# Optimization experiments

Hardware: AMD Instinct MI355X
Metric: run time of the kernel (lower is better)

## Reference

```python
import jax, jax.numpy as jnp
import numpy as np

DIM = 768
HEADS = 12
DIM_HEAD = 64
INNER = HEADS * DIM_HEAD
L = 256
EPS = 1e-08


def setup_inputs() -> dict:
    key = jax.random.key(0)
    k1, k2, k3, k4 = jax.random.split(key, 4)
    x = jax.random.normal(k1, (2, 4096, DIM), dtype=jnp.float32)
    # Linear weights stored torch-style: (out_features, in_features)
    w_qkv = jax.random.normal(k2, (3 * INNER, DIM), dtype=jnp.float32) * (DIM ** -0.5)
    w_out = jax.random.normal(k3, (DIM, INNER), dtype=jnp.float32) * (INNER ** -0.5)
    b_out = jax.random.normal(k4, (DIM,), dtype=jnp.float32) * 0.01
    # learned per-head log-scale temperature, init log2(L^2 - L)
    scale = jnp.full((HEADS,), np.log2(L * L - L), dtype=jnp.float32)
    return {"x": x, "w_qkv": w_qkv, "w_out": w_out, "b_out": b_out, "scale": scale}


def reference(x, w_qkv, w_out, b_out, scale):
    b, n, d = x.shape
    h, dh = HEADS, DIM_HEAD
    qkv = x @ w_qkv.T                                   # [b, n, 3*inner]
    q, k, v = jnp.split(qkv, 3, axis=-1)
    # [b, n, h, dh] -> [b, h, n, dh]
    q, k, v = (t.reshape(b, n, h, dh).transpose(0, 2, 1, 3) for t in (q, k, v))
    # Faithful to source: L2 norm over the HEADS axis (dim=1), then rsqrt
    q = q * jax.lax.rsqrt(jnp.linalg.norm(q, axis=1, keepdims=True) + EPS)
    k = k * jax.lax.rsqrt(jnp.linalg.norm(k, axis=1, keepdims=True) + EPS)
    dots = jnp.einsum('bhid,bhjd->bhij', q, k)          # [b, h, n, n]
    scores = jax.nn.softmax(dots / scale[:, None, None], axis=-1)
    out = jnp.einsum('bhij,bhjd->bhid', scores, v)      # [b, h, n, dh]
    out = out.transpose(0, 2, 1, 3).reshape(b, n, h * dh)
    return out @ w_out.T + b_out
```

## Files before the change

kernel.cpp:

```cpp
#include <hip/hip_runtime.h>
#include <hip/hip_bf16.h>

#define DIMX   768
#define HEADS  12
#define DH     64
#define INNER  768
#define NQKV   2304
#define SEQ    4096
#define BATCH  2
#define ROWS   (BATCH*SEQ)
#define EPSF   1e-8f
#define LOG2E  1.4426950408889634f

typedef __bf16 bf16x8 __attribute__((ext_vector_type(8)));
typedef float  f32x4  __attribute__((ext_vector_type(4)));
typedef float  f32x16 __attribute__((ext_vector_type(16)));
typedef unsigned u32x2 __attribute__((ext_vector_type(2)));

__device__ __forceinline__ unsigned short f2bf(float f) {
    unsigned int u = __float_as_uint(f);
    unsigned int r = ((u >> 16) & 1u) + 0x7FFFu;
    return (unsigned short)((u + r) >> 16);
}
__device__ __forceinline__ float bf2f(unsigned short u) {
    return __builtin_bit_cast(float, (unsigned)u << 16);
}
__device__ __forceinline__ unsigned pkbf(float a, float b) {
    unsigned short la = __builtin_bit_cast(unsigned short, (__bf16)a);
    unsigned short lb = __builtin_bit_cast(unsigned short, (__bf16)b);
    return (unsigned)la | ((unsigned)lb << 16);
}

__device__ __forceinline__ void gload_lds16(const void* g, void* l) {
    __builtin_amdgcn_global_load_lds(
        (const __attribute__((address_space(1))) void*)g,
        (__attribute__((address_space(3))) void*)l, 16, 0, 0);
}

__global__ __launch_bounds__(256) void cast_f32_bf16(
    const float* __restrict__ src, unsigned short* __restrict__ dst, int n)
{
    int i = (blockIdx.x * 256 + threadIdx.x) * 4;
    if (i + 3 < n) {
        float4 v = *reinterpret_cast<const float4*>(src + i);
        ushort4 o;
        o.x = f2bf(v.x); o.y = f2bf(v.y); o.z = f2bf(v.z); o.w = f2bf(v.w);
        *reinterpret_cast<ushort4*>(dst + i) = o;
    }
}

template<bool BF16OUT>
__global__ __launch_bounds__(256) void gemm_bt_kernel(
    const unsigned short* __restrict__ A,
    const unsigned short* __restrict__ B,
    void* __restrict__ Cv,
    const float* __restrict__ bias,
    int M, int N, int K, int bmx)
{
    __shared__ unsigned short shA[128][64];
    __shared__ unsigned short shB[128][64];

    const int xcd = blockIdx.x & 7;
    const int idx = blockIdx.x >> 3;
    const int bm0 = (xcd * bmx + (idx % bmx)) * 128;
    const int bn0 = (idx / bmx) * 128;
    const int tid = threadIdx.x;
    const int lane = tid & 63;
    const int wid  = tid >> 6;
    const int l15  = lane & 15;
    const int l4   = lane >> 4;
    const int wr   = wid >> 1;
    const int wc   = wid & 1;
    const int srow = lane >> 3;
    const int scol = (lane & 7) * 8;

    f32x4 acc[4][4];
    #pragma unroll
    for (int i = 0; i < 4; ++i)
        #pragma unroll
        for (int j = 0; j < 4; ++j)
            acc[i][j] = (f32x4){0.f, 0.f, 0.f, 0.f};

    const int nkt = K >> 6;
    for (int kt = 0; kt < nkt; ++kt) {
        const int k0 = kt << 6;
        __syncthreads();
        #pragma unroll
        for (int j = 0; j < 4; ++j) {
            int row = wid * 32 + j * 8;
            gload_lds16(&A[(size_t)(bm0 + row + srow) * K + k0 + scol], &shA[row][0]);
            gload_lds16(&B[(size_t)(bn0 + row + srow) * K + k0 + scol], &shB[row][0]);
        }
        __syncthreads();
        #pragma unroll
        for (int ks = 0; ks < 2; ++ks) {
            bf16x8 af[4], bfr[4];
            #pragma unroll
            for (int mf = 0; mf < 4; ++mf)
                af[mf] = *reinterpret_cast<const bf16x8*>(&shA[wr * 64 + mf * 16 + l15][ks * 32 + l4 * 8]);
            #pragma unroll
            for (int nf = 0; nf < 4; ++nf)
                bfr[nf] = *reinterpret_cast<const bf16x8*>(&shB[wc * 64 + nf * 16 + l15][ks * 32 + l4 * 8]);
            #pragma unroll
            for (int mf = 0; mf < 4; ++mf)
                #pragma unroll
                for (int nf = 0; nf < 4; ++nf)
                    acc[mf][nf] = __builtin_amdgcn_mfma_f32_16x16x32_bf16(
                        af[mf], bfr[nf], acc[mf][nf], 0, 0, 0);
        }
    }

    #pragma unroll
    for (int mf = 0; mf < 4; ++mf) {
        #pragma unroll
        for (int nf = 0; nf < 4; ++nf) {
            int col = bn0 + wc * 64 + nf * 16 + l15;
            float badd = bias ? bias[col] : 0.f;
            #pragma unroll
            for (int r = 0; r < 4; ++r) {
                int row = bm0 + wr * 64 + mf * 16 + l4 * 4 + r;
                if constexpr (BF16OUT)
                    ((unsigned short*)Cv)[(size_t)row * N + col] = f2bf(acc[mf][nf][r] + badd);
                else
                    ((float*)Cv)[(size_t)row * N + col] = acc[mf][nf][r] + badd;
            }
        }
    }
}

__global__ __launch_bounds__(256) void normalize_kernel(
    const unsigned short* __restrict__ qkv,
    const float* __restrict__ scale,
    unsigned short* __restrict__ qo,
    unsigned short* __restrict__ ko)
{
    int t = blockIdx.x * 256 + threadIdx.x;
    int row = t >> 6;
    int d = t & 63;
    int b = row >> 12;
    int n = row & 4095;
    const unsigned short* base = qkv + (size_t)row * NQKV;

    float qv[12], kv[12];
    float sq = 0.f, sk = 0.f;
    #pragma unroll
    for (int h = 0; h < 12; ++h) {
        qv[h] = bf2f(base[h * 64 + d]);
        kv[h] = bf2f(base[768 + h * 64 + d]);
        sq += qv[h] * qv[h];
        sk += kv[h] * kv[h];
    }
    float rq = rsqrtf(sqrtf(sq) + EPSF);
    float rk = rsqrtf(sqrtf(sk) + EPSF);
    #pragma unroll
    for (int h = 0; h < 12; ++h) {
        size_t bh = (size_t)(b * 12 + h);
        float fold = LOG2E / scale[h];
        qo[(bh * SEQ + n) * 64 + d] = f2bf(qv[h] * rq * fold);
        ko[(bh * SEQ + n) * 64 + d] = f2bf(kv[h] * rk);
    }
}

__global__ __launch_bounds__(256) void vtrans_kernel(
    const unsigned short* __restrict__ qkv,
    unsigned short* __restrict__ vt)
{
    __shared__ unsigned short tile[64][72];
    const int bh = blockIdx.x;
    const int nt = blockIdx.y;
    const int b = bh / HEADS, h = bh % HEADS;
    const int tid = threadIdx.x;

    #pragma unroll
    for (int it = 0; it < 2; ++it) {
        int c = tid + it * 256;
        int r = c >> 3, cc = c & 7;
        *reinterpret_cast<uint4*>(&tile[r][cc * 8]) =
            *reinterpret_cast<const uint4*>(
                &qkv[(size_t)(b * SEQ + nt * 64 + r) * NQKV + 1536 + h * 64 + cc * 8]);
    }
    __syncthreads();
    #pragma unroll
    for (int it = 0; it < 2; ++it) {
        int c = tid + it * 256;
        int d = c >> 3, nc = c & 7;
        ushort4 o0, o1;
        o0.x = tile[nc * 8 + 0][d]; o0.y = tile[nc * 8 + 1][d];
        o0.z = tile[nc * 8 + 2][d]; o0.w = tile[nc * 8 + 3][d];
        o1.x = tile[nc * 8 + 4][d]; o1.y = tile[nc * 8 + 5][d];
        o1.z = tile[nc * 8 + 6][d]; o1.w = tile[nc * 8 + 7][d];
        unsigned short* dst = &vt[((size_t)bh * 64 + d) * SEQ + nt * 64 + nc * 8];
        *reinterpret_cast<ushort4*>(dst)     = o0;
        *reinterpret_cast<ushort4*>(dst + 4) = o1;
    }
}

__global__ __launch_bounds__(256) void attn_kernel(
    const unsigned short* __restrict__ qg,
    const unsigned short* __restrict__ kg,
    const unsigned short* __restrict__ vtg,
    unsigned short* __restrict__ attnout)
{
    __shared__ unsigned short shK[64][72];
    __shared__ unsigned short shV[64][72];

    const int wg   = blockIdx.x;
    const int xcd  = wg & 7;
    const int slot = wg >> 3;
    const int bh   = xcd * 3 + (slot >> 5);
    const int qblk = slot & 31;
    const int b    = bh / HEADS;
    const int h    = bh % HEADS;

    const int tid  = threadIdx.x;
    const int lane = tid & 63;
    const int wid  = tid >> 6;
    const int l31  = lane & 31;
    const int hi   = lane >> 5;

    bf16x8 qf[4];
    {
        const unsigned short* qrow =
            qg + ((size_t)bh * SEQ + qblk * 128 + wid * 32 + l31) * 64 + hi * 8;
        #pragma unroll
        for (int d0 = 0; d0 < 4; ++d0)
            qf[d0] = *reinterpret_cast<const bf16x8*>(qrow + d0 * 16);
    }

    f32x16 ot[2];
    #pragma unroll
    for (int r = 0; r < 16; ++r) { ot[0][r] = 0.f; ot[1][r] = 0.f; }
    float l_lane = 0.f;

    const unsigned short* kbase = kg  + (size_t)bh * SEQ * 64;
    const unsigned short* vbase = vtg + (size_t)bh * 64 * SEQ;

    for (int kt = 0; kt < SEQ / 64; ++kt) {
        __syncthreads();
        #pragma unroll
        for (int it = 0; it < 2; ++it) {
            int c = tid + it * 256;
            int row = c >> 3, colc = c & 7;
            *reinterpret_cast<uint4*>(&shK[row][colc * 8]) =
                *reinterpret_cast<const uint4*>(&kbase[(size_t)(kt * 64 + row) * 64 + colc * 8]);
            *reinterpret_cast<uint4*>(&shV[row][colc * 8]) =
                *reinterpret_cast<const uint4*>(&vbase[(size_t)row * SEQ + kt * 64 + colc * 8]);
        }
        __syncthreads();

        f32x16 st0, st1;
        #pragma unroll
        for (int r = 0; r < 16; ++r) { st0[r] = 0.f; st1[r] = 0.f; }
        __builtin_amdgcn_s_setprio(1);
        #pragma unroll
        for (int d0 = 0; d0 < 4; ++d0) {
            bf16x8 kf0 = *reinterpret_cast<const bf16x8*>(&shK[l31][d0 * 16 + hi * 8]);
            bf16x8 kf1 = *reinterpret_cast<const bf16x8*>(&shK[32 + l31][d0 * 16 + hi * 8]);
            st0 = __builtin_amdgcn_mfma_f32_32x32x16_bf16(kf0, qf[d0], st0, 0, 0, 0);
            st1 = __builtin_amdgcn_mfma_f32_32x32x16_bf16(kf1, qf[d0], st1, 0, 0, 0);
        }
        __builtin_amdgcn_s_setprio(0);

        float s0 = 0.f, s1 = 0.f, s2 = 0.f, s3 = 0.f;
        unsigned cp0[8], cp1[8];
        #pragma unroll
        for (int t = 0; t < 8; ++t) {
            float pa = __builtin_amdgcn_exp2f(st0[2 * t]);
            float pb = __builtin_amdgcn_exp2f(st0[2 * t + 1]);
            float pc = __builtin_amdgcn_exp2f(st1[2 * t]);
            float pd = __builtin_amdgcn_exp2f(st1[2 * t + 1]);
            s0 += pa; s1 += pb; s2 += pc; s3 += pd;
            cp0[t] = pkbf(pa, pb);
            cp1[t] = pkbf(pc, pd);
        }
        l_lane += (s0 + s1) + (s2 + s3);

        __builtin_amdgcn_s_setprio(1);
        #pragma unroll
        for (int cb = 0; cb < 2; ++cb) {
            #pragma unroll
            for (int kk = 0; kk < 2; ++kk) {
                unsigned c0 = cb ? cp1[4 * kk + 0] : cp0[4 * kk + 0];
                unsigned c1 = cb ? cp1[4 * kk + 1] : cp0[4 * kk + 1];
                unsigned c2 = cb ? cp1[4 * kk + 2] : cp0[4 * kk + 2];
                unsigned c3 = cb ? cp1[4 * kk + 3] : cp0[4 * kk + 3];
                u32x2 s = __builtin_amdgcn_permlane32_swap(c0, c2, false, false);
                u32x2 t = __builtin_amdgcn_permlane32_swap(c1, c3, false, false);
                union { unsigned uu[4]; bf16x8 v; } pu;
                pu.uu[0] = s.x;
                pu.uu[1] = t.x;
                pu.uu[2] = s.y;
                pu.uu[3] = t.y;
                #pragma unroll
                for (int df = 0; df < 2; ++df) {
                    bf16x8 vf = *reinterpret_cast<const bf16x8*>(
                        &shV[df * 32 + l31][cb * 32 + kk * 16 + hi * 8]);
                    ot[df] = __builtin_amdgcn_mfma_f32_32x32x16_bf16(vf, pu.v, ot[df], 0, 0, 0);
                }
            }
        }
        __builtin_amdgcn_s_setprio(0);
    }

    float l_all = l_lane + __shfl_xor(l_lane, 32);
    float invl = 1.0f / l_all;
    int n = qblk * 128 + wid * 32 + l31;
    unsigned short* orow = attnout + ((size_t)(b * SEQ + n)) * INNER + h * 64;
    #pragma unroll
    for (int df = 0; df < 2; ++df) {
        #pragma unroll
        for (int t = 0; t < 4; ++t) {
            unsigned w0 = pkbf(ot[df][4 * t]     * invl, ot[df][4 * t + 1] * invl);
            unsigned w1 = pkbf(ot[df][4 * t + 2] * invl, ot[df][4 * t + 3] * invl);
            unsigned long long pk = (unsigned long long)w0 | ((unsigned long long)w1 << 32);
            *reinterpret_cast<unsigned long long*>(orow + df * 32 + t * 8 + hi * 4) = pk;
        }
    }
}

extern "C" void kernel_launch(void* const* d_in, const int* in_sizes, int n_in,
                              void* d_out, int out_size, void* d_ws, size_t ws_size,
                              hipStream_t stream)
{
    const float* x      = (const float*)d_in[0];
    const float* w_qkv  = (const float*)d_in[1];
    const float* w_out  = (const float*)d_in[2];
    const float* b_out  = (const float*)d_in[3];
    const float* scale  = (const float*)d_in[4];
    float* out = (float*)d_out;
    char* ws = (char*)d_ws;

    unsigned short* xb    = (unsigned short*)(ws);
    unsigned short* wqkvb = (unsigned short*)(ws + 12582912);
    unsigned short* woutb = (unsigned short*)(ws + 16121856);
    unsigned short* attnb = (unsigned short*)(ws + 17301504);
    unsigned short* qb    = (unsigned short*)(ws + 29884416);
    unsigned short* kb    = (unsigned short*)(ws + 42467328);
    unsigned short* vtb   = (unsigned short*)(ws + 55050240);
    unsigned short* qkvb  = (unsigned short*)(ws + 67633152);

    cast_f32_bf16<<<6144, 256, 0, stream>>>(x, xb, 6291456);
    cast_f32_bf16<<<1728, 256, 0, stream>>>(w_qkv, wqkvb, 1769472);
    cast_f32_bf16<<<576, 256, 0, stream>>>(w_out, woutb, 589824);

    gemm_bt_kernel<true><<<1152, 256, 0, stream>>>(xb, wqkvb, qkvb, nullptr, ROWS, NQKV, DIMX, 8);

    normalize_kernel<<<2048, 256, 0, stream>>>(qkvb, scale, qb, kb);
    vtrans_kernel<<<dim3(BATCH * HEADS, SEQ / 64), 256, 0, stream>>>(qkvb, vtb);

    attn_kernel<<<768, 256, 0, stream>>>(qb, kb, vtb, attnb);

    gemm_bt_kernel<false><<<384, 256, 0, stream>>>(attnb, woutb, out, b_out, ROWS, INNER, INNER, 8);
}
```

Baseline: 267.1 us.

## Load K/V MFMA fragments directly from global memory, dropping LDS staging

The attention loop no longer stages K and V^T tiles in shared memory behind two barriers per iteration. Each wave now loads its own K and V MFMA fragments straight from global memory into registers, and the setprio hints are removed. This removes LDS traffic and block-wide synchronisation. In exchange, each of the 4 waves loads the same K/V tiles redundantly from global/L2, register pressure rises, and load latency is exposed without explicit prefetching.

```diff
diff --git a/kernel.cpp b/kernel.cpp
--- a/kernel.cpp
+++ b/kernel.cpp
@@ -201,9 +201,6 @@
     const unsigned short* __restrict__ vtg,
     unsigned short* __restrict__ attnout)
 {
-    __shared__ unsigned short shK[64][72];
-    __shared__ unsigned short shV[64][72];
-
     const int wg   = blockIdx.x;
     const int xcd  = wg & 7;
     const int slot = wg >> 3;
@@ -232,34 +229,34 @@
     for (int r = 0; r < 16; ++r) { ot[0][r] = 0.f; ot[1][r] = 0.f; }
     float l_lane = 0.f;
 
-    const unsigned short* kbase = kg  + (size_t)bh * SEQ * 64;
-    const unsigned short* vbase = vtg + (size_t)bh * 64 * SEQ;
+    const unsigned short* krow0 = kg + ((size_t)bh * SEQ + l31) * 64 + hi * 8;
+    const unsigned short* krow1 = krow0 + (size_t)32 * 64;
+    const unsigned short* vrow0 = vtg + ((size_t)bh * 64 + l31) * SEQ + hi * 8;
+    const unsigned short* vrow1 = vrow0 + (size_t)32 * SEQ;
 
     for (int kt = 0; kt < SEQ / 64; ++kt) {
-        __syncthreads();
-        #pragma unroll
-        for (int it = 0; it < 2; ++it) {
-            int c = tid + it * 256;
-            int row = c >> 3, colc = c & 7;
-            *reinterpret_cast<uint4*>(&shK[row][colc * 8]) =
-                *reinterpret_cast<const uint4*>(&kbase[(size_t)(kt * 64 + row) * 64 + colc * 8]);
-            *reinterpret_cast<uint4*>(&shV[row][colc * 8]) =
-                *reinterpret_cast<const uint4*>(&vbase[(size_t)row * SEQ + kt * 64 + colc * 8]);
-        }
-        __syncthreads();
+        bf16x8 kf0[4], kf1[4];
+        #pragma unroll
+        for (int d0 = 0; d0 < 4; ++d0) {
+            kf0[d0] = *reinterpret_cast<const bf16x8*>(krow0 + (size_t)kt * 64 * 64 + d0 * 16);
+            kf1[d0] = *reinterpret_cast<const bf16x8*>(krow1 + (size_t)kt * 64 * 64 + d0 * 16);
+        }
 
         f32x16 st0, st1;
         #pragma unroll
         for (int r = 0; r < 16; ++r) { st0[r] = 0.f; st1[r] = 0.f; }
-        __builtin_amdgcn_s_setprio(1);
         #pragma unroll
         for (int d0 = 0; d0 < 4; ++d0) {
-            bf16x8 kf0 = *reinterpret_cast<const bf16x8*>(&shK[l31][d0 * 16 + hi * 8]);
-            bf16x8 kf1 = *reinterpret_cast<const bf16x8*>(&shK[32 + l31][d0 * 16 + hi * 8]);
-            st0 = __builtin_amdgcn_mfma_f32_32x32x16_bf16(kf0, qf[d0], st0, 0, 0, 0);
-            st1 = __builtin_amdgcn_mfma_f32_32x32x16_bf16(kf1, qf[d0], st1, 0, 0, 0);
-        }
-        __builtin_amdgcn_s_setprio(0);
+            st0 = __builtin_amdgcn_mfma_f32_32x32x16_bf16(kf0[d0], qf[d0], st0, 0, 0, 0);
+            st1 = __builtin_amdgcn_mfma_f32_32x32x16_bf16(kf1[d0], qf[d0], st1, 0, 0, 0);
+        }
+
+        bf16x8 vf0[4], vf1[4];
+        #pragma unroll
+        for (int j = 0; j < 4; ++j) {
+            vf0[j] = *reinterpret_cast<const bf16x8*>(vrow0 + kt * 64 + j * 16);
+            vf1[j] = *reinterpret_cast<const bf16x8*>(vrow1 + kt * 64 + j * 16);
+        }
 
         float s0 = 0.f, s1 = 0.f, s2 = 0.f, s3 = 0.f;
         unsigned cp0[8], cp1[8];
@@ -275,7 +272,6 @@
         }
         l_lane += (s0 + s1) + (s2 + s3);
 
-        __builtin_amdgcn_s_setprio(1);
         #pragma unroll
         for (int cb = 0; cb < 2; ++cb) {
             #pragma unroll
@@ -291,15 +287,11 @@
                 pu.uu[1] = t.x;
                 pu.uu[2] = s.y;
                 pu.uu[3] = t.y;
-                #pragma unroll
-                for (int df = 0; df < 2; ++df) {
-                    bf16x8 vf = *reinterpret_cast<const bf16x8*>(
-                        &shV[df * 32 + l31][cb * 32 + kk * 16 + hi * 8]);
-                    ot[df] = __builtin_amdgcn_mfma_f32_32x32x16_bf16(vf, pu.v, ot[df], 0, 0, 0);
-                }
+                const int j = cb * 2 + kk;
+                ot[0] = __builtin_amdgcn_mfma_f32_32x32x16_bf16(vf0[j], pu.v, ot[0], 0, 0, 0);
+                ot[1] = __builtin_amdgcn_mfma_f32_32x32x16_bf16(vf1[j], pu.v, ot[1], 0, 0, 0);
             }
         }
-        __builtin_amdgcn_s_setprio(0);
     }
 
     float l_all = l_lane + __shfl_xor(l_lane, 32);
```

New measurement: 462.3 us. +73.1%, slower.

## Prefetch next K/V tile into registers during attention compute

Applied to the files above, without the earlier changes.

Moves the global loads of the next K and V tile into registers at the start of each iteration, so they are in flight while the QK and PV MFMAs and the softmax exps run. The registers are written to shared memory after compute, between two barriers. It also removes the s_setprio priority hints around the MFMA sections. The cost is more registers held live through the loop, which can reduce occupancy.

```diff
diff --git a/kernel.cpp b/kernel.cpp
--- a/kernel.cpp
+++ b/kernel.cpp
@@ -217,6 +217,8 @@
     const int wid  = tid >> 6;
     const int l31  = lane & 31;
     const int hi   = lane >> 5;
+    const int r0 = tid >> 3;
+    const int sc = (tid & 7) * 8;
 
     bf16x8 qf[4];
     {
@@ -235,23 +237,33 @@
     const unsigned short* kbase = kg  + (size_t)bh * SEQ * 64;
     const unsigned short* vbase = vtg + (size_t)bh * 64 * SEQ;
 
+    {
+        uint4 rk0 = *reinterpret_cast<const uint4*>(&kbase[(size_t)r0 * 64 + sc]);
+        uint4 rk1 = *reinterpret_cast<const uint4*>(&kbase[(size_t)(32 + r0) * 64 + sc]);
+        uint4 rv0 = *reinterpret_cast<const uint4*>(&vbase[(size_t)r0 * SEQ + sc]);
+        uint4 rv1 = *reinterpret_cast<const uint4*>(&vbase[(size_t)(32 + r0) * SEQ + sc]);
+        *reinterpret_cast<uint4*>(&shK[r0][sc])      = rk0;
+        *reinterpret_cast<uint4*>(&shK[32 + r0][sc]) = rk1;
+        *reinterpret_cast<uint4*>(&shV[r0][sc])      = rv0;
+        *reinterpret_cast<uint4*>(&shV[32 + r0][sc]) = rv1;
+    }
+    __syncthreads();
+
     for (int kt = 0; kt < SEQ / 64; ++kt) {
-        __syncthreads();
-        #pragma unroll
-        for (int it = 0; it < 2; ++it) {
-            int c = tid + it * 256;
-            int row = c >> 3, colc = c & 7;
-            *reinterpret_cast<uint4*>(&shK[row][colc * 8]) =
-                *reinterpret_cast<const uint4*>(&kbase[(size_t)(kt * 64 + row) * 64 + colc * 8]);
-            *reinterpret_cast<uint4*>(&shV[row][colc * 8]) =
-                *reinterpret_cast<const uint4*>(&vbase[(size_t)row * SEQ + kt * 64 + colc * 8]);
-        }
-        __syncthreads();
+        uint4 rk0, rk1, rv0, rv1;
+        const bool more = (kt < SEQ / 64 - 1);
+        if (more) {
+            const unsigned short* kn = kbase + (size_t)(kt + 1) * 64 * 64;
+            const unsigned short* vn = vbase + (size_t)(kt + 1) * 64;
+            rk0 = *reinterpret_cast<const uint4*>(&kn[(size_t)r0 * 64 + sc]);
+            rk1 = *reinterpret_cast<const uint4*>(&kn[(size_t)(32 + r0) * 64 + sc]);
+            rv0 = *reinterpret_cast<const uint4*>(&vn[(size_t)r0 * SEQ + sc]);
+            rv1 = *reinterpret_cast<const uint4*>(&vn[(size_t)(32 + r0) * SEQ + sc]);
+        }
 
         f32x16 st0, st1;
         #pragma unroll
         for (int r = 0; r < 16; ++r) { st0[r] = 0.f; st1[r] = 0.f; }
-        __builtin_amdgcn_s_setprio(1);
         #pragma unroll
         for (int d0 = 0; d0 < 4; ++d0) {
             bf16x8 kf0 = *reinterpret_cast<const bf16x8*>(&shK[l31][d0 * 16 + hi * 8]);
@@ -259,7 +271,6 @@
             st0 = __builtin_amdgcn_mfma_f32_32x32x16_bf16(kf0, qf[d0], st0, 0, 0, 0);
             st1 = __builtin_amdgcn_mfma_f32_32x32x16_bf16(kf1, qf[d0], st1, 0, 0, 0);
         }
-        __builtin_amdgcn_s_setprio(0);
 
         float s0 = 0.f, s1 = 0.f, s2 = 0.f, s3 = 0.f;
         unsigned cp0[8], cp1[8];
@@ -275,7 +286,6 @@
         }
         l_lane += (s0 + s1) + (s2 + s3);
 
-        __builtin_amdgcn_s_setprio(1);
         #pragma unroll
         for (int cb = 0; cb < 2; ++cb) {
             #pragma unroll
@@ -299,7 +309,15 @@
                 }
             }
         }
-        __builtin_amdgcn_s_setprio(0);
+
+        __syncthreads();
+        if (more) {
+            *reinterpret_cast<uint4*>(&shK[r0][sc])      = rk0;
+            *reinterpret_cast<uint4*>(&shK[32 + r0][sc]) = rk1;
+            *reinterpret_cast<uint4*>(&shV[r0][sc])      = rv0;
+            *reinterpret_cast<uint4*>(&shV[32 + r0][sc]) = rv1;
+        }
+        __syncthreads();
     }
 
     float l_all = l_lane + __shfl_xor(l_lane, 32);
```

After: 266.3 us. Within noise of the previous version (-0.3%).
